# Kernel optimization log

Hardware: AMD Instinct MI355X
Metric: run time of the kernel (lower is better)

Reference implementation:

```python
import jax, jax.numpy as jnp
import numpy as np

SEC = 20  # keypoints per section (hard-coded in original: i*20:(i+1)*20)


def smooth_l1(x):
    ax = jnp.abs(x)
    return jnp.where(ax < 1.0, 0.5 * x * x, ax - 0.5)


def setup_inputs() -> dict:
    key = jax.random.key(0)
    k1, k2, k3, k4 = jax.random.split(key, 4)
    B, K, NS = 8192, 400, 20
    return {
        "pred_keypoints": jax.random.normal(k1, (B, K, 3), dtype=jnp.float32),
        "gt_keypoints": jax.random.normal(k2, (B, K, 3), dtype=jnp.float32),
        "pred_section_logits": jax.random.normal(k3, (B, K, NS), dtype=jnp.float32),
        "gt_section_label": jax.random.randint(k4, (B, K), 0, NS, dtype=jnp.int64),
    }


def reference(pred_keypoints, gt_keypoints, pred_section_logits, gt_section_label):
    alpha, beta, delta, epsilon = 1.0, 4.0, 5.0, 6.0
    B, K, _ = pred_keypoints.shape
    S = K // SEC  # num sections

    keypoint_loss = jnp.mean(smooth_l1(pred_keypoints - gt_keypoints))

    # cross entropy over flattened [B*K, NS]
    logp = jax.nn.log_softmax(pred_section_logits, axis=-1)
    nll = -jnp.take_along_axis(logp, gt_section_label[..., None], axis=-1)[..., 0]
    section_loss = jnp.mean(nll)

    # per-section Procrustes alignment, batched over (B, S)
    P = pred_keypoints.reshape(B, S, SEC, 3)
    G = gt_keypoints.reshape(B, S, SEC, 3)
    Pc = P - P.mean(axis=2, keepdims=True)
    Gc = G - G.mean(axis=2, keepdims=True)
    # H = gt_centered^T @ pred_centered -> [B, S, 3, 3]
    H = jnp.einsum('bski,bskj->bsij', Gc, Pc)
    U, _, Vh = jnp.linalg.svd(H)  # torch.svd gives V with H = U diag(s) V^T; Vh = V^T
    R = jnp.einsum('bsik,bskj->bsij', U, Vh)  # U @ V^T
    P_aligned = jnp.einsum('bski,bsij->bskj', Pc, R)
    # sum of per-section means / S == overall mean (equal-size sections)
    rot_loss = jnp.mean(smooth_l1(P_aligned - Gc))

    # center alignment loss
    cent_loss = jnp.mean(smooth_l1(P.mean(axis=2) - G.mean(axis=2)))

    total = alpha * section_loss + beta * keypoint_loss + delta * rot_loss + epsilon * cent_loss
    return total
```

## Files before the change

### kernel.cpp

```cpp
#include <hip/hip_runtime.h>
#include <math.h>

static constexpr int Bn    = 8192;
static constexpr int Kn    = 400;
static constexpr int Sn    = 20;
static constexpr int NROWS = Bn * Kn;
static constexpr int NGRP  = Bn * Sn;

static constexpr int CE_BLOCKS = 2560, CE_TPB = 256, CE_RPT = 5;
static constexpr int PR_BLOCKS = 640,  PR_TPB = 256;
static constexpr int FUSED_BLOCKS = CE_BLOCKS + PR_BLOCKS;

static constexpr int WS_CE   = 0;
static constexpr int WS_KP   = 4096;
static constexpr int WS_ROT  = 8192;
static constexpr int WS_CENT = 12288;

__device__ __forceinline__ float smooth_l1f(float x) {
    float ax = fabsf(x);
    return ax < 1.0f ? 0.5f * x * x : ax - 0.5f;
}

__global__ __launch_bounds__(256) void fused_kernel(
    const float* __restrict__ logits,
    const int*   __restrict__ labels,
    const float* __restrict__ P,
    const float* __restrict__ G,
    float*       __restrict__ ws)
{
    const int t   = threadIdx.x;
    const int bid = blockIdx.x;
    const int lane = t & 63, wid = t >> 6;
    __shared__ float sm[3][4];

    if ((bid % 5) != 4) {
        const int cb = (bid / 5) * 4 + (bid % 5);
        const size_t tid  = (size_t)cb * CE_TPB + t;
        const size_t row0 = tid * CE_RPT;
        const float4* __restrict__ src = reinterpret_cast<const float4*>(logits) + row0 * 5;

        float acc = 0.0f;
#pragma unroll
        for (int r = 0; r < CE_RPT; r++) {
            float x[20];
#pragma unroll
            for (int i = 0; i < 5; i++) {
                float4 v = src[r * 5 + i];
                x[4*i+0] = v.x; x[4*i+1] = v.y; x[4*i+2] = v.z; x[4*i+3] = v.w;
            }
            int lab = labels[row0 + r];
            float m = x[0];
#pragma unroll
            for (int j = 1; j < 20; j++) m = fmaxf(m, x[j]);
            float se = 0.0f, xl = 0.0f;
#pragma unroll
            for (int j = 0; j < 20; j++) {
                se += __expf(x[j] - m);
                xl = (j == lab) ? x[j] : xl;
            }
            acc += __logf(se) + m - xl;
        }

#pragma unroll
        for (int o = 32; o > 0; o >>= 1) acc += __shfl_down(acc, o);
        if (lane == 0) sm[0][wid] = acc;
        __syncthreads();
        if (t == 0) ws[WS_CE + cb] = sm[0][0] + sm[0][1] + sm[0][2] + sm[0][3];
        return;
    }

    const int pb  = bid / 5;
    const int grp = pb * PR_TPB + t;
    const float4* __restrict__ pp = reinterpret_cast<const float4*>(P) + (size_t)grp * 15;
    const float4* __restrict__ gg = reinterpret_cast<const float4*>(G) + (size_t)grp * 15;

    float kp = 0.0f;
    float sp[3] = {0,0,0}, sg[3] = {0,0,0};
#pragma unroll
    for (int i = 0; i < 15; i++) {
        float4 a = pp[i], b = gg[i];
        float av[4] = {a.x, a.y, a.z, a.w};
        float bv[4] = {b.x, b.y, b.z, b.w};
#pragma unroll
        for (int j = 0; j < 4; j++) {
            int c = (4*i + j) % 3;
            kp += smooth_l1f(av[j] - bv[j]);
            sp[c] += av[j]; sg[c] += bv[j];
        }
    }
    const float inv20 = 1.0f / 20.0f;
    float mp[3] = {sp[0]*inv20, sp[1]*inv20, sp[2]*inv20};
    float mg[3] = {sg[0]*inv20, sg[1]*inv20, sg[2]*inv20};
    float cent = smooth_l1f(mp[0]-mg[0]) + smooth_l1f(mp[1]-mg[1]) + smooth_l1f(mp[2]-mg[2]);

    float X[3][3] = {{0,0,0},{0,0,0},{0,0,0}};
#pragma unroll
    for (int ch = 0; ch < 5; ch++) {
        float4 a0 = pp[3*ch+0], a1 = pp[3*ch+1], a2 = pp[3*ch+2];
        float4 b0 = gg[3*ch+0], b1 = gg[3*ch+1], b2 = gg[3*ch+2];
        float pv[12] = {a0.x,a0.y,a0.z,a0.w, a1.x,a1.y,a1.z,a1.w, a2.x,a2.y,a2.z,a2.w};
        float gv[12] = {b0.x,b0.y,b0.z,b0.w, b1.x,b1.y,b1.z,b1.w, b2.x,b2.y,b2.z,b2.w};
#pragma unroll
        for (int q = 0; q < 4; q++) {
            float pc0 = pv[3*q+0]-mp[0], pc1 = pv[3*q+1]-mp[1], pc2 = pv[3*q+2]-mp[2];
            float gc0 = gv[3*q+0]-mg[0], gc1 = gv[3*q+1]-mg[1], gc2 = gv[3*q+2]-mg[2];
            X[0][0] += gc0*pc0; X[0][1] += gc0*pc1; X[0][2] += gc0*pc2;
            X[1][0] += gc1*pc0; X[1][1] += gc1*pc1; X[1][2] += gc1*pc2;
            X[2][0] += gc2*pc0; X[2][1] += gc2*pc1; X[2][2] += gc2*pc2;
        }
    }

#pragma unroll
    for (int it = 0; it < 8; it++) {
        float c00 =  X[1][1]*X[2][2] - X[1][2]*X[2][1];
        float c01 = -(X[1][0]*X[2][2] - X[1][2]*X[2][0]);
        float c02 =  X[1][0]*X[2][1] - X[1][1]*X[2][0];
        float c10 = -(X[0][1]*X[2][2] - X[0][2]*X[2][1]);
        float c11 =  X[0][0]*X[2][2] - X[0][2]*X[2][0];
        float c12 = -(X[0][0]*X[2][1] - X[0][1]*X[2][0]);
        float c20 =  X[0][1]*X[1][2] - X[0][2]*X[1][1];
        float c21 = -(X[0][0]*X[1][2] - X[0][2]*X[1][0]);
        float c22 =  X[0][0]*X[1][1] - X[0][1]*X[1][0];
        float d = X[0][0]*c00 + X[0][1]*c01 + X[0][2]*c02;
        float ad = fmaxf(fabsf(d), 1e-30f);
        float gam = __powf(ad, -(1.0f/3.0f));
        float dsn = (d < 0.0f) ? -ad : ad;
        float k1 = 0.5f * gam;
        float k2 = 0.5f / (gam * dsn);
        X[0][0] = k1*X[0][0] + k2*c00;  X[0][1] = k1*X[0][1] + k2*c01;  X[0][2] = k1*X[0][2] + k2*c02;
        X[1][0] = k1*X[1][0] + k2*c10;  X[1][1] = k1*X[1][1] + k2*c11;  X[1][2] = k1*X[1][2] + k2*c12;
        X[2][0] = k1*X[2][0] + k2*c20;  X[2][1] = k1*X[2][1] + k2*c21;  X[2][2] = k1*X[2][2] + k2*c22;
    }
    float s9 = X[0][0]+X[0][1]+X[0][2]+X[1][0]+X[1][1]+X[1][2]+X[2][0]+X[2][1]+X[2][2];
    if (!(s9 == s9) || fabsf(s9) > 1e10f) {
        X[0][0]=1; X[0][1]=0; X[0][2]=0;
        X[1][0]=0; X[1][1]=1; X[1][2]=0;
        X[2][0]=0; X[2][1]=0; X[2][2]=1;
    }

    float rot = 0.0f;
#pragma unroll
    for (int ch = 0; ch < 5; ch++) {
        float4 a0 = pp[3*ch+0], a1 = pp[3*ch+1], a2 = pp[3*ch+2];
        float4 b0 = gg[3*ch+0], b1 = gg[3*ch+1], b2 = gg[3*ch+2];
        float pv[12] = {a0.x,a0.y,a0.z,a0.w, a1.x,a1.y,a1.z,a1.w, a2.x,a2.y,a2.z,a2.w};
        float gv[12] = {b0.x,b0.y,b0.z,b0.w, b1.x,b1.y,b1.z,b1.w, b2.x,b2.y,b2.z,b2.w};
#pragma unroll
        for (int q = 0; q < 4; q++) {
            float pc0 = pv[3*q+0]-mp[0], pc1 = pv[3*q+1]-mp[1], pc2 = pv[3*q+2]-mp[2];
            float gc0 = gv[3*q+0]-mg[0], gc1 = gv[3*q+1]-mg[1], gc2 = gv[3*q+2]-mg[2];
            float a0r = pc0*X[0][0] + pc1*X[1][0] + pc2*X[2][0] - gc0;
            float a1r = pc0*X[0][1] + pc1*X[1][1] + pc2*X[2][1] - gc1;
            float a2r = pc0*X[0][2] + pc1*X[1][2] + pc2*X[2][2] - gc2;
            rot += smooth_l1f(a0r) + smooth_l1f(a1r) + smooth_l1f(a2r);
        }
    }

#pragma unroll
    for (int o = 32; o > 0; o >>= 1) {
        kp   += __shfl_down(kp, o);
        rot  += __shfl_down(rot, o);
        cent += __shfl_down(cent, o);
    }
    if (lane == 0) { sm[0][wid] = kp; sm[1][wid] = rot; sm[2][wid] = cent; }
    __syncthreads();
    if (t == 0) {
        ws[WS_KP   + pb] = sm[0][0] + sm[0][1] + sm[0][2] + sm[0][3];
        ws[WS_ROT  + pb] = sm[1][0] + sm[1][1] + sm[1][2] + sm[1][3];
        ws[WS_CENT + pb] = sm[2][0] + sm[2][1] + sm[2][2] + sm[2][3];
    }
}

__global__ __launch_bounds__(256) void reduce_kernel(
    const float* __restrict__ ws, float* __restrict__ out)
{
    const int t = threadIdx.x;
    float s_ce = 0, s_kp = 0, s_rot = 0, s_cent = 0;
    for (int i = t; i < CE_BLOCKS; i += 256) s_ce += ws[WS_CE + i];
    for (int i = t; i < PR_BLOCKS; i += 256) {
        s_kp   += ws[WS_KP + i];
        s_rot  += ws[WS_ROT + i];
        s_cent += ws[WS_CENT + i];
    }
#pragma unroll
    for (int o = 32; o > 0; o >>= 1) {
        s_ce   += __shfl_down(s_ce, o);
        s_kp   += __shfl_down(s_kp, o);
        s_rot  += __shfl_down(s_rot, o);
        s_cent += __shfl_down(s_cent, o);
    }
    __shared__ float sm[4][4];
    int lane = t & 63, wid = t >> 6;
    if (lane == 0) { sm[0][wid]=s_ce; sm[1][wid]=s_kp; sm[2][wid]=s_rot; sm[3][wid]=s_cent; }
    __syncthreads();
    if (t == 0) {
        float ce   = (sm[0][0]+sm[0][1]+sm[0][2]+sm[0][3]) * (1.0f / (float)NROWS);
        float kp   = (sm[1][0]+sm[1][1]+sm[1][2]+sm[1][3]) * (1.0f / (float)(NROWS * 3));
        float rot  = (sm[2][0]+sm[2][1]+sm[2][2]+sm[2][3]) * (1.0f / (float)(NROWS * 3));
        float cent = (sm[3][0]+sm[3][1]+sm[3][2]+sm[3][3]) * (1.0f / (float)(NGRP * 3));
        out[0] = ce + 4.0f * kp + 5.0f * rot + 6.0f * cent;
    }
}

extern "C" void kernel_launch(void* const* d_in, const int* in_sizes, int n_in,
                              void* d_out, int out_size, void* d_ws, size_t ws_size,
                              hipStream_t stream) {
    const float* pred_kp = (const float*)d_in[0];
    const float* gt_kp   = (const float*)d_in[1];
    const float* logits  = (const float*)d_in[2];
    const int*   labels  = (const int*)d_in[3];
    float* out = (float*)d_out;
    float* ws  = (float*)d_ws;

    fused_kernel<<<FUSED_BLOCKS, 256, 0, stream>>>(logits, labels, pred_kp, gt_kp, ws);
    reduce_kernel<<<1, 256, 0, stream>>>(ws, out);
}
```

Measured before the change: 451.9 us.

## Stage CE logits through double-buffered LDS and fuse Procrustes stats into one pass

The cross-entropy blocks now load logits cooperatively with lane-contiguous float4 accesses into a double-buffered shared-memory tile, prefetching the next chunk while computing the current one. This replaces the per-thread strided 80-byte row reads, which coalesced poorly. The Procrustes path computes the sums and the raw cross-covariance in a single pass and then applies the mean correction algebraically, removing one global read pass. The cost is 40KB of LDS per block, which lowers occupancy, and a slight loss of numerical precision from the uncentred covariance.

```diff
diff --git a/kernel.cpp b/kernel.cpp
--- a/kernel.cpp
+++ b/kernel.cpp
@@ -7,7 +7,8 @@
 static constexpr int NROWS = Bn * Kn;
 static constexpr int NGRP  = Bn * Sn;
 
-static constexpr int CE_BLOCKS = 2560, CE_TPB = 256, CE_RPT = 5;
+static constexpr int CE_BLOCKS = 2560;
+static constexpr int CE_ROWS_PER_BLOCK = 1280;
 static constexpr int PR_BLOCKS = 640,  PR_TPB = 256;
 static constexpr int FUSED_BLOCKS = CE_BLOCKS + PR_BLOCKS;
 
@@ -31,24 +32,43 @@
     const int t   = threadIdx.x;
     const int bid = blockIdx.x;
     const int lane = t & 63, wid = t >> 6;
+    __shared__ float lbuf[2][5120];
     __shared__ float sm[3][4];
 
     if ((bid % 5) != 4) {
         const int cb = (bid / 5) * 4 + (bid % 5);
-        const size_t tid  = (size_t)cb * CE_TPB + t;
-        const size_t row0 = tid * CE_RPT;
-        const float4* __restrict__ src = reinterpret_cast<const float4*>(logits) + row0 * 5;
+        const size_t blockRow0 = (size_t)cb * CE_ROWS_PER_BLOCK;
+        const float* __restrict__ gsrc = logits + blockRow0 * 20;
+
+        float4 pf[5];
+        auto load_chunk = [&](int c) {
+            const float* p = gsrc + (size_t)c * 5120 + wid * 1280 + lane * 4;
+#pragma unroll
+            for (int i = 0; i < 5; i++)
+                pf[i] = *reinterpret_cast<const float4*>(p + i * 256);
+        };
+        auto store_chunk = [&](int buf) {
+#pragma unroll
+            for (int i = 0; i < 5; i++)
+                *reinterpret_cast<float4*>(&lbuf[buf][wid * 1280 + i * 256 + lane * 4]) = pf[i];
+        };
+
+        load_chunk(0);
+        store_chunk(0);
 
         float acc = 0.0f;
 #pragma unroll
-        for (int r = 0; r < CE_RPT; r++) {
+        for (int c = 0; c < 5; c++) {
+            if (c + 1 < 5) load_chunk(c + 1);
+
+            const float4* rowp = reinterpret_cast<const float4*>(&lbuf[c & 1][t * 20]);
             float x[20];
 #pragma unroll
             for (int i = 0; i < 5; i++) {
-                float4 v = src[r * 5 + i];
+                float4 v = rowp[i];
                 x[4*i+0] = v.x; x[4*i+1] = v.y; x[4*i+2] = v.z; x[4*i+3] = v.w;
             }
-            int lab = labels[row0 + r];
+            int lab = labels[blockRow0 + c * 256 + t];
             float m = x[0];
 #pragma unroll
             for (int j = 1; j < 20; j++) m = fmaxf(m, x[j]);
@@ -59,6 +79,8 @@
                 xl = (j == lab) ? x[j] : xl;
             }
             acc += __logf(se) + m - xl;
+
+            if (c + 1 < 5) store_chunk((c + 1) & 1);
         }
 
 #pragma unroll
@@ -75,25 +97,8 @@
     const float4* __restrict__ gg = reinterpret_cast<const float4*>(G) + (size_t)grp * 15;
 
     float kp = 0.0f;
-    float sp[3] = {0,0,0}, sg[3] = {0,0,0};
-#pragma unroll
-    for (int i = 0; i < 15; i++) {
-        float4 a = pp[i], b = gg[i];
-        float av[4] = {a.x, a.y, a.z, a.w};
-        float bv[4] = {b.x, b.y, b.z, b.w};
-#pragma unroll
-        for (int j = 0; j < 4; j++) {
-            int c = (4*i + j) % 3;
-            kp += smooth_l1f(av[j] - bv[j]);
-            sp[c] += av[j]; sg[c] += bv[j];
-        }
-    }
-    const float inv20 = 1.0f / 20.0f;
-    float mp[3] = {sp[0]*inv20, sp[1]*inv20, sp[2]*inv20};
-    float mg[3] = {sg[0]*inv20, sg[1]*inv20, sg[2]*inv20};
-    float cent = smooth_l1f(mp[0]-mg[0]) + smooth_l1f(mp[1]-mg[1]) + smooth_l1f(mp[2]-mg[2]);
-
-    float X[3][3] = {{0,0,0},{0,0,0},{0,0,0}};
+    float sp0=0,sp1=0,sp2=0, sg0=0,sg1=0,sg2=0;
+    float S00=0,S01=0,S02=0, S10=0,S11=0,S12=0, S20=0,S21=0,S22=0;
 #pragma unroll
     for (int ch = 0; ch < 5; ch++) {
         float4 a0 = pp[3*ch+0], a1 = pp[3*ch+1], a2 = pp[3*ch+2];
@@ -102,13 +107,25 @@
         float gv[12] = {b0.x,b0.y,b0.z,b0.w, b1.x,b1.y,b1.z,b1.w, b2.x,b2.y,b2.z,b2.w};
 #pragma unroll
         for (int q = 0; q < 4; q++) {
-            float pc0 = pv[3*q+0]-mp[0], pc1 = pv[3*q+1]-mp[1], pc2 = pv[3*q+2]-mp[2];
-            float gc0 = gv[3*q+0]-mg[0], gc1 = gv[3*q+1]-mg[1], gc2 = gv[3*q+2]-mg[2];
-            X[0][0] += gc0*pc0; X[0][1] += gc0*pc1; X[0][2] += gc0*pc2;
-            X[1][0] += gc1*pc0; X[1][1] += gc1*pc1; X[1][2] += gc1*pc2;
-            X[2][0] += gc2*pc0; X[2][1] += gc2*pc1; X[2][2] += gc2*pc2;
+            float p0 = pv[3*q+0], p1 = pv[3*q+1], p2 = pv[3*q+2];
+            float g0 = gv[3*q+0], g1 = gv[3*q+1], g2 = gv[3*q+2];
+            kp += smooth_l1f(p0-g0) + smooth_l1f(p1-g1) + smooth_l1f(p2-g2);
+            sp0 += p0; sp1 += p1; sp2 += p2;
+            sg0 += g0; sg1 += g1; sg2 += g2;
+            S00 += g0*p0; S01 += g0*p1; S02 += g0*p2;
+            S10 += g1*p0; S11 += g1*p1; S12 += g1*p2;
+            S20 += g2*p0; S21 += g2*p1; S22 += g2*p2;
         }
     }
+    const float inv20 = 1.0f / 20.0f;
+    float mp[3] = {sp0*inv20, sp1*inv20, sp2*inv20};
+    float mg[3] = {sg0*inv20, sg1*inv20, sg2*inv20};
+    float cent = smooth_l1f(mp[0]-mg[0]) + smooth_l1f(mp[1]-mg[1]) + smooth_l1f(mp[2]-mg[2]);
+
+    float X[3][3];
+    X[0][0] = S00 - 20.0f*mg[0]*mp[0];  X[0][1] = S01 - 20.0f*mg[0]*mp[1];  X[0][2] = S02 - 20.0f*mg[0]*mp[2];
+    X[1][0] = S10 - 20.0f*mg[1]*mp[0];  X[1][1] = S11 - 20.0f*mg[1]*mp[1];  X[1][2] = S12 - 20.0f*mg[1]*mp[2];
+    X[2][0] = S20 - 20.0f*mg[2]*mp[0];  X[2][1] = S21 - 20.0f*mg[2]*mp[1];  X[2][2] = S22 - 20.0f*mg[2]*mp[2];
 
 #pragma unroll
     for (int it = 0; it < 8; it++) {
```

Result: faster. 440.3 us (-2.6%).
